# Kernel tuning notes

Measured on AMD Instinct MI355X. Metric: run time of the kernel, lower is better.

## Reference

```python
import jax, jax.numpy as jnp
import numpy as np

B, S, H, V, C = 32, 512, 256, 50000, 5
NUM_LAYERS, WINDOW = 2, 2


def setup_inputs() -> dict:
    key = jax.random.key(0)
    ks = jax.random.split(key, 24)
    std = 0.1  # matches nn.init.normal_(p, 0, 0.1)
    n = lambda k, shp: jax.random.normal(k, shp, dtype=jnp.float32) * std
    u = lambda k, shp: -0.05 + jax.random.uniform(k, shp, dtype=jnp.float32) * 0.1
    return {
        "input_sentences": jax.random.randint(ks[0], (B, S), 0, V),
        "sentences_length": jax.random.randint(ks[1], (B,), 1, S),
        "hh0": u(ks[2], (B, S, H)),
        "cs0": u(ks[3], (B, S, H)),
        "embed": n(ks[4], (V, H)),
        # stacked word-gate weights, gate order: i, l, r, f, s, output, u
        "W_lr": n(ks[5], (7, H, 2 * H)),
        "W_c": n(ks[6], (7, H, H)),
        "W_x": n(ks[7], (7, H, H)),
        "W_g": n(ks[8], (7, H, H)),
        "gate_bias": n(ks[9], (7, H)),
        # sentence-state gates
        "W_fg_g": n(ks[10], (H, H)),
        "W_fg_h": n(ks[11], (H, H)),
        "W_fgi_g": n(ks[12], (H, H)),
        "W_fgi_h": n(ks[13], (H, H)),
        "W_og_g": n(ks[14], (H, H)),
        "W_og_h": n(ks[15], (H, H)),
        "b_fg": n(ks[16], (H,)),
        "b_fgi": n(ks[17], (H,)),
        # output head
        "W1": n(ks[18], (H, 2 * H)),
        "b1": n(ks[19], (H,)),
        "Wout": n(ks[20], (C, H)),
        "bout": n(ks[21], (C,)),
    }


def _before_sum(x, window):
    # sum of right-shifted (zero-padded at front) copies, shifts 1..window
    out = jnp.zeros_like(x)
    for s in range(1, window + 1):
        out = out + jnp.pad(x[:, :-s], ((0, 0), (s, 0), (0, 0)))
    return out


def _after_sum(x, window):
    out = jnp.zeros_like(x)
    for s in range(1, window + 1):
        out = out + jnp.pad(x[:, s:], ((0, 0), (0, s), (0, 0)))
    return out


def _slstm_step(hh, cs, sv, scs, wv, W_lr, W_c, W_x, W_g, gate_bias,
                W_fg_g, W_fg_h, W_fgi_g, W_fgi_h, W_og_g, W_og_h, b_fg, b_fgi):
    avg_hh = hh.mean(axis=1)                                   # [B,H]
    f_hat_g = jax.nn.sigmoid(sv @ W_fg_g.T + avg_hh @ W_fg_h.T + b_fg)
    # NOTE: original code (faithfully) uses output_gate_bias here, not output_gate_g_bias
    og_g = jax.nn.sigmoid(sv @ W_og_g.T + avg_hh @ W_og_h.T + gate_bias[5])
    f_hat_g_i = jax.nn.sigmoid((sv @ W_fgi_g.T)[:, None] + hh @ W_fgi_h.T + b_fgi)
    scores = jax.nn.softmax(f_hat_g_i, axis=2)                 # over hidden dim
    new_scs = jax.nn.softmax(f_hat_g, axis=1) * scs + (scores * cs).sum(axis=1)
    new_sv = og_g * jnp.tanh(new_scs)

    hb = _before_sum(hh, WINDOW)
    ha = _after_sum(hh, WINDOW)
    cb = _before_sum(cs, WINDOW)
    ca = _after_sum(cs, WINDOW)
    ba = jnp.concatenate([hb, ha], axis=-1)                    # [B,S,2H]

    # all 7 gate pre-activations at once: [B,S,7,H]
    pre = (jnp.einsum('bsk,ghk->bsgh', ba, W_lr)
           + jnp.einsum('bsk,ghk->bsgh', hh, W_c)
           + jnp.einsum('bsk,ghk->bsgh', wv, W_x)
           + (jnp.einsum('bk,ghk->bgh', new_sv, W_g) + gate_bias)[:, None])

    g5 = jax.nn.sigmoid(pre[..., :5, :])                       # i,l,r,f,s
    b_, s_ = g5.shape[:2]
    # joint softmax over the concatenated 5*H gate vector (as in torch cat+softmax)
    g5 = jax.nn.softmax(g5.reshape(b_, s_, -1), axis=-1).reshape(b_, s_, 5, -1)
    i_t, l_t, r_t, f_t, s_t = (g5[..., k, :] for k in range(5))
    og = jax.nn.sigmoid(pre[..., 5, :])
    u_g = jnp.tanh(pre[..., 6, :])

    new_cs = l_t * cb + f_t * cs + r_t * ca + s_t * scs[:, None] + i_t * u_g
    new_hh = og * jnp.tanh(new_cs)
    return new_hh, new_cs, new_sv, new_scs


def reference(input_sentences, sentences_length, hh0, cs0, embed,
              W_lr, W_c, W_x, W_g, gate_bias,
              W_fg_g, W_fg_h, W_fgi_g, W_fgi_h, W_og_g, W_og_h, b_fg, b_fgi,
              W1, b1, Wout, bout):
    wv = embed[input_sentences]                                # [B,S,H]
    hh, cs = hh0, cs0
    sv, scs = hh0.mean(axis=1), cs0.mean(axis=1)
    for _ in range(NUM_LAYERS):
        hh, cs, sv, scs = _slstm_step(hh, cs, sv, scs, wv,
                                      W_lr, W_c, W_x, W_g, gate_bias,
                                      W_fg_g, W_fg_h, W_fgi_g, W_fgi_h,
                                      W_og_g, W_og_h, b_fg, b_fgi)
    avg_hh = hh.mean(axis=1)
    conc = jnp.concatenate([avg_hh, sv], axis=1) @ W1.T + b1
    fc = conc @ Wout.T + bout
    return jax.nn.log_softmax(fc, axis=1), sv
```

## Files before the change

### kernel.cpp

```cpp
#include <hip/hip_runtime.h>
#include <stdint.h>
#include <math.h>

#define B_   32
#define S_   512
#define H_   256
#define M_   (B_*S_)
#define KBIG 1024
#define NB   1792
#define C_   5

typedef __bf16 bf16;
typedef __bf16 bf16x8 __attribute__((ext_vector_type(8)));
typedef float  floatx4 __attribute__((ext_vector_type(4)));

__device__ __forceinline__ float sigm(float x){ return 1.f/(1.f+expf(-x)); }

__device__ __forceinline__ void gl16(const bf16* g, bf16* l){
    __builtin_amdgcn_global_load_lds(
        (const __attribute__((address_space(1))) unsigned int*)g,
        (__attribute__((address_space(3))) unsigned int*)l, 16, 0, 0);
}

__global__ void wcomb_k(const float* __restrict__ Wlr, const float* __restrict__ Wc,
                        const float* __restrict__ Wx, bf16* __restrict__ WT){
    int n = blockIdx.x;
    int g = n >> 8, h = n & 255;
    int k4 = threadIdx.x * 4;
    const float* src;
    if (k4 < 512)      src = Wlr + ((size_t)(g*256 + h))*512 + k4;
    else if (k4 < 768) src = Wc  + ((size_t)(g*256 + h))*256 + (k4 - 512);
    else               src = Wx  + ((size_t)(g*256 + h))*256 + (k4 - 768);
    float4 v = *(const float4*)src;
    bf16 o[4] = {(bf16)v.x,(bf16)v.y,(bf16)v.z,(bf16)v.w};
    *(uint2*)&WT[(size_t)n*KBIG + k4] = *(uint2*)o;
}

__global__ void cvtw_k(const float* __restrict__ a, bf16* __restrict__ o){
    int i4 = (blockIdx.x*256 + threadIdx.x)*4;
    float4 v = *(const float4*)(a + i4);
    bf16 t[4] = {(bf16)v.x,(bf16)v.y,(bf16)v.z,(bf16)v.w};
    *(uint2*)(o + i4) = *(uint2*)t;
}

__global__ void gather_k(const int* __restrict__ idx, const float* __restrict__ embed,
                         bf16* __restrict__ wv){
    int i4 = (blockIdx.x*256 + threadIdx.x)*4;
    int m = i4 >> 8, h = i4 & 255;
    float4 v = *(const float4*)(embed + (size_t)idx[m]*H_ + h);
    bf16 o[4] = {(bf16)v.x,(bf16)v.y,(bf16)v.z,(bf16)v.w};
    *(uint2*)(wv + (size_t)m*H_ + h) = *(uint2*)o;
}

__global__ void mean1_k(const float* __restrict__ x, float* __restrict__ part){
    int b = blockIdx.x, c = blockIdx.y, h = threadIdx.x;
    const float* p = x + ((size_t)b*S_ + c*32)*H_ + h;
    float s = 0.f;
    #pragma unroll 8
    for (int t=0;t<32;t++) s += p[(size_t)t*H_];
    part[((size_t)b*16 + c)*H_ + h] = s;
}
__global__ void mean2_k(const float* __restrict__ part, float* __restrict__ out){
    int b = blockIdx.x, h = threadIdx.x;
    float s = 0.f;
    #pragma unroll
    for (int c=0;c<16;c++) s += part[((size_t)b*16 + c)*H_ + h];
    out[b*H_ + h] = s * (1.f/512.f);
}

__global__ void buildx_k(const float* __restrict__ hh, const bf16* __restrict__ wv,
                         bf16* __restrict__ X){
    int m = blockIdx.x, h = threadIdx.x;
    int s = m & (S_-1);
    size_t base = (size_t)m*H_ + h;
    float hb = (s>=1    ? hh[base - H_] : 0.f) + (s>=2    ? hh[base - 2*H_] : 0.f);
    float ha = (s<=S_-2 ? hh[base + H_] : 0.f) + (s<=S_-3 ? hh[base + 2*H_] : 0.f);
    bf16* xr = X + (size_t)m*KBIG;
    xr[h]     = (bf16)hb;
    xr[256+h] = (bf16)ha;
    xr[512+h] = (bf16)hh[base];
    xr[768+h] = wv[base];
}

__global__ void mv5_k(const float* __restrict__ sv, const float* __restrict__ avg,
    const float* __restrict__ Wfg_g, const float* __restrict__ Wfg_h,
    const float* __restrict__ Wog_g, const float* __restrict__ Wog_h,
    const float* __restrict__ Wfgi_g, float* __restrict__ res){
    int j = blockIdx.x, b = blockIdx.y, h = threadIdx.x;
    const float* vec = (j==1 || j==3) ? avg + b*H_ : sv + b*H_;
    const float* W   = (j==0)?Wfg_g:(j==1)?Wfg_h:(j==2)?Wog_g:(j==3)?Wog_h:Wfgi_g;
    __shared__ float v[H_];
    v[h] = vec[h]; __syncthreads();
    const float* w = W + (size_t)h*H_;
    float d = 0.f;
    for (int k=0;k<H_;k++) d += v[k]*w[k];
    res[((size_t)b*5 + j)*H_ + h] = d;
}
__global__ void comb_k(const float* __restrict__ res, const float* __restrict__ b_fg,
                       const float* __restrict__ gbias, const float* __restrict__ b_fgi,
                       float* __restrict__ fhg, float* __restrict__ ogg,
                       float* __restrict__ svg){
    int b = blockIdx.x, h = threadIdx.x;
    const float* r = res + (size_t)b*5*H_;
    fhg[b*H_+h] = sigm(r[h] + r[H_+h] + b_fg[h]);
    ogg[b*H_+h] = sigm(r[2*H_+h] + r[3*H_+h] + gbias[5*H_+h]);
    svg[b*H_+h] = r[4*H_+h] + b_fgi[h];
}

template<int EPI>
__global__ __launch_bounds__(256)
void mgemm_k(const bf16* __restrict__ A, const bf16* __restrict__ BT,
             bf16* __restrict__ C, const float* __restrict__ gt,
             int Kdim, int lda, int ldb, int ldc){
    __shared__ alignas(16) bf16 lsA[128*32];
    __shared__ alignas(16) bf16 lsB[128*32];
    int tid  = threadIdx.x;
    int m0 = blockIdx.y * 128, n0 = blockIdx.x * 128;
    int wave = tid >> 6, lane = tid & 63;
    int wm = (wave & 1) * 64, wn = (wave >> 1) * 64;
    int lrow = lane & 15, quad = lane >> 4;

    floatx4 zero = {0.f,0.f,0.f,0.f};
    floatx4 acc[4][4];
    #pragma unroll
    for (int i=0;i<4;i++)
        #pragma unroll
        for (int j=0;j<4;j++) acc[i][j] = zero;

    int srow = tid >> 2;
    int scol = (tid & 3) * 8;
    const bf16* Abase = A  + (size_t)(m0 + srow)*lda + scol;
    const bf16* Bbase = BT + (size_t)(n0 + srow)*ldb + scol;
    bf16* dA0 = &lsA[srow*32 + scol];
    bf16* dA1 = &lsA[(64+srow)*32 + scol];
    bf16* dB0 = &lsB[srow*32 + scol];
    bf16* dB1 = &lsB[(64+srow)*32 + scol];

    for (int k0 = 0; k0 < Kdim; k0 += 32){
        __syncthreads();
        gl16(Abase + k0,                     dA0);
        gl16(Abase + (size_t)64*lda + k0,    dA1);
        gl16(Bbase + k0,                     dB0);
        gl16(Bbase + (size_t)64*ldb + k0,    dB1);
        __syncthreads();
        bf16x8 af[4], bfr[4];
        #pragma unroll
        for (int mi=0;mi<4;mi++) af[mi]  = *(const bf16x8*)&lsA[(wm+mi*16+lrow)*32 + quad*8];
        #pragma unroll
        for (int ni=0;ni<4;ni++) bfr[ni] = *(const bf16x8*)&lsB[(wn+ni*16+lrow)*32 + quad*8];
        #pragma unroll
        for (int mi=0;mi<4;mi++)
            #pragma unroll
            for (int ni=0;ni<4;ni++)
                acc[mi][ni] = __builtin_amdgcn_mfma_f32_16x16x32_bf16(af[mi], bfr[ni], acc[mi][ni], 0, 0, 0);
    }

    #pragma unroll
    for (int mi=0;mi<4;mi++)
        #pragma unroll
        for (int ni=0;ni<4;ni++){
            int row = m0 + wm + mi*16 + quad*4;
            int col = n0 + wn + ni*16 + lrow;
            #pragma unroll
            for (int r=0;r<4;r++){
                float v = acc[mi][ni][r];
                if (EPI) v += gt[(size_t)((row+r)>>9)*NB + col];
                C[(size_t)(row+r)*ldc + col] = (bf16)v;
            }
        }
}

template<int EPI>
__device__ __forceinline__ void mmq(floatx4 (&acc)[8][4], bf16x8 (&af)[4][2], bf16x8 (&bfr)[2][2],
                                    int MH, int NH){
    #pragma unroll
    for (int mi2=0;mi2<4;mi2++)
        #pragma unroll
        for (int ni2=0;ni2<2;ni2++)
            #pragma unroll
            for (int kk=0;kk<2;kk++)
                acc[MH*4+mi2][NH*2+ni2] = __builtin_amdgcn_mfma_f32_16x16x32_bf16(
                    af[mi2][kk], bfr[ni2][kk], acc[MH*4+mi2][NH*2+ni2], 0, 0, 0);
}

template<int EPI>
__global__ __launch_bounds__(512, 2)
void mgemm256_k(const bf16* __restrict__ A, const bf16* __restrict__ BT,
                bf16* __restrict__ C, const float* __restrict__ gt,
                int Kdim, int lda, int ldb, int ldc){
    __shared__ alignas(16) bf16 lsA[2][256*64];
    __shared__ alignas(16) bf16 lsB[2][256*64];
    const int tid  = threadIdx.x;
    const int lane = tid & 63;
    const int wave = tid >> 6;
    const int wm = wave >> 2;
    const int wn = wave & 3;
    const int lrow = lane & 15, quad = lane >> 4;
    const int m0 = blockIdx.y * 256, n0 = blockIdx.x * 256;

    const int srow = tid >> 3;
    const int scol = ((tid & 7) ^ (srow & 7)) * 8;
    const bf16* Ab = A  + (size_t)(m0 + srow)*lda + scol;
    const bf16* Bb = BT + (size_t)(n0 + srow)*ldb + scol;
    const int NT = Kdim >> 6;

    floatx4 zero = {0.f,0.f,0.f,0.f};
    floatx4 acc[8][4];
    #pragma unroll
    for (int i=0;i<8;i++)
        #pragma unroll
        for (int j=0;j<4;j++) acc[i][j] = zero;
    bf16x8 af[4][2], bfr[2][2];

#define SA_(bu,r,kt) gl16(Ab + (size_t)(r)*64*lda + (size_t)(kt)*64, &lsA[bu][(r)*4096 + tid*8])
#define SB_(bu,r,kt) gl16(Bb + (size_t)(r)*64*ldb + (size_t)(kt)*64, &lsB[bu][(r)*4096 + tid*8])
#define RA_(bu,MH,mi2,kk) (*(const bf16x8*)&lsA[bu][(wm*128 + (MH)*64 + (mi2)*16 + lrow)*64 + ((((kk)*4+quad) ^ (lrow&7))*8)])
#define RB_(bu,NH,ni2,kk) (*(const bf16x8*)&lsB[bu][(wn*64  + (NH)*32 + (ni2)*16 + lrow)*64 + ((((kk)*4+quad) ^ (lrow&7))*8)])

    SB_(0,0,0); SB_(0,1,0); SB_(0,2,0); SB_(0,3,0);
    SA_(0,0,0); SA_(0,2,0); SA_(0,1,0); SA_(0,3,0);
    asm volatile("s_waitcnt vmcnt(2)" ::: "memory");
    __builtin_amdgcn_s_barrier();

    #pragma unroll 2
    for (int kt = 0; kt < NT; ++kt){
        const int cur = kt & 1, nxt = cur ^ 1;
        const bool st = (kt + 1 < NT);
        const int k1 = kt + 1;

        if (st){ SB_(nxt,0,k1); SB_(nxt,1,k1); }
        #pragma unroll
        for (int mi2=0;mi2<4;mi2++){ af[mi2][0] = RA_(cur,0,mi2,0); af[mi2][1] = RA_(cur,0,mi2,1); }
        #pragma unroll
        for (int ni2=0;ni2<2;ni2++){ bfr[ni2][0] = RB_(cur,0,ni2,0); bfr[ni2][1] = RB_(cur,0,ni2,1); }
        __builtin_amdgcn_s_barrier();
        __builtin_amdgcn_s_setprio(1);
        mmq<EPI>(acc, af, bfr, 0, 0);
        __builtin_amdgcn_s_setprio(0);
        __builtin_amdgcn_s_barrier();

        if (st){ SB_(nxt,2,k1); SB_(nxt,3,k1); }
        #pragma unroll
        for (int ni2=0;ni2<2;ni2++){ bfr[ni2][0] = RB_(cur,1,ni2,0); bfr[ni2][1] = RB_(cur,1,ni2,1); }
        __builtin_amdgcn_s_barrier();
        __builtin_amdgcn_s_setprio(1);
        mmq<EPI>(acc, af, bfr, 0, 1);
        __builtin_amdgcn_s_setprio(0);
        if (st) asm volatile("s_waitcnt vmcnt(4)" ::: "memory");
        else    asm volatile("s_waitcnt vmcnt(0)" ::: "memory");
        __builtin_amdgcn_s_barrier();

        if (st){ SA_(nxt,0,k1); SA_(nxt,2,k1); }
        #pragma unroll
        for (int mi2=0;mi2<4;mi2++){ af[mi2][0] = RA_(cur,1,mi2,0); af[mi2][1] = RA_(cur,1,mi2,1); }
        __builtin_amdgcn_s_barrier();
        __builtin_amdgcn_s_setprio(1);
        mmq<EPI>(acc, af, bfr, 1, 1);
        __builtin_amdgcn_s_setprio(0);
        __builtin_amdgcn_s_barrier();

        if (st){ SA_(nxt,1,k1); SA_(nxt,3,k1); }
        #pragma unroll
        for (int ni2=0;ni2<2;ni2++){ bfr[ni2][0] = RB_(cur,0,ni2,0); bfr[ni2][1] = RB_(cur,0,ni2,1); }
        __builtin_amdgcn_s_barrier();
        __builtin_amdgcn_s_setprio(1);
        mmq<EPI>(acc, af, bfr, 1, 0);
        __builtin_amdgcn_s_setprio(0);
        asm volatile("s_waitcnt vmcnt(2)" ::: "memory");
        __builtin_amdgcn_s_barrier();
    }
#undef SA_
#undef SB_
#undef RA_
#undef RB_

    float gtv[4] = {0.f,0.f,0.f,0.f};
    if (EPI){
        const int b = m0 >> 9;
        #pragma unroll
        for (int ni=0;ni<4;ni++)
            gtv[ni] = gt[(size_t)b*NB + n0 + wn*64 + ni*16 + lrow];
    }
    #pragma unroll
    for (int mi=0;mi<8;mi++)
        #pragma unroll
        for (int ni=0;ni<4;ni++){
            int row = m0 + wm*128 + mi*16 + quad*4;
            int col = n0 + wn*64  + ni*16 + lrow;
            #pragma unroll
            for (int r=0;r<4;r++){
                float v = acc[mi][ni][r];
                if (EPI) v += gtv[ni];
                C[(size_t)(row+r)*ldc + col] = (bf16)v;
            }
        }
}

__global__ void scorep_k(const bf16* __restrict__ fgih, const float* __restrict__ svg,
                         const float* __restrict__ cs, float* __restrict__ part){
    int chunk = blockIdx.x, b = blockIdx.y;
    int tid = threadIdx.x, wave = tid >> 6, lane = tid & 63;
    __shared__ float acc4[4][256];
    float sw[4], acc[4] = {0.f,0.f,0.f,0.f};
    #pragma unroll
    for (int j=0;j<4;j++) sw[j] = svg[b*H_ + lane + 64*j];
    for (int t=wave; t<16; t+=4){
        int m = b*S_ + chunk*16 + t;
        const bf16* fr = fgih + (size_t)m*H_;
        float e[4], loc = 0.f;
        #pragma unroll
        for (int j=0;j<4;j++){ e[j] = expf(sigm(sw[j] + (float)fr[lane+64*j])); loc += e[j]; }
        #pragma unroll
        for (int off=32; off; off>>=1) loc += __shfl_xor(loc, off, 64);
        float inv = 1.f/loc;
        const float* cr = cs + (size_t)m*H_;
        #pragma unroll
        for (int j=0;j<4;j++) acc[j] += e[j]*inv*cr[lane+64*j];
    }
    #pragma unroll
    for (int j=0;j<4;j++) acc4[wave][lane+64*j] = acc[j];
    __syncthreads();
    part[((size_t)b*32 + chunk)*H_ + tid] =
        acc4[0][tid] + acc4[1][tid] + acc4[2][tid] + acc4[3][tid];
}

__global__ void newscs_k(const float* __restrict__ part, const float* __restrict__ fhg,
                         const float* __restrict__ ogg, const float* __restrict__ scs_in,
                         float* __restrict__ scs_out, float* __restrict__ sv_out){
    int b = blockIdx.x, h = threadIdx.x;
    __shared__ float r[256];
    float dot = 0.f;
    #pragma unroll 8
    for (int c=0;c<32;c++) dot += part[((size_t)b*32+c)*H_ + h];
    float e = expf(fhg[b*H_+h]);
    r[h] = e; __syncthreads();
    for (int off=128; off; off>>=1){ if (h<off) r[h] += r[h+off]; __syncthreads(); }
    float ns = (e / r[0]) * scs_in[b*H_+h] + dot;
    scs_out[b*H_+h] = ns;
    sv_out[b*H_+h]  = ogg[b*H_+h] * tanhf(ns);
}

__global__ void gterm_k(const float* __restrict__ svn, const float* __restrict__ Wg,
                        const float* __restrict__ gbias, float* __restrict__ gt){
    int g = blockIdx.x, b = blockIdx.y, h = threadIdx.x;
    __shared__ float s[H_];
    s[h] = svn[b*H_+h]; __syncthreads();
    const float* w = Wg + ((size_t)g*H_ + h)*H_;
    float d = 0.f;
    for (int k=0;k<H_;k++) d += s[k]*w[k];
    gt[(size_t)b*NB + g*H_ + h] = d + gbias[g*H_+h];
}

__global__ void gates_k(const bf16* __restrict__ pre, const float* __restrict__ cs_in,
                        const float* __restrict__ scs_in,
                        float* __restrict__ hh_out, float* __restrict__ cs_out){
    int tid = threadIdx.x, wave = tid >> 6, lane = tid & 63;
    int m = blockIdx.x*4 + wave;
    int b = m >> 9, s = m & (S_-1);
    const bf16* row = pre + (size_t)m*NB;
    float ex[4][5], og[4], u[4];
    float loc = 0.f;
    #pragma unroll
    for (int j=0;j<4;j++){
        int h = lane + 64*j;
        #pragma unroll
        for (int g=0; g<5; ++g){
            float e = expf(sigm((float)row[g*H_ + h]));
            ex[j][g] = e; loc += e;
        }
        og[j] = sigm((float)row[5*H_ + h]);
        u[j]  = tanhf((float)row[6*H_ + h]);
    }
    #pragma unroll
    for (int off=32; off; off>>=1) loc += __shfl_xor(loc, off, 64);
    float inv = 1.f / loc;
    #pragma unroll
    for (int j=0;j<4;j++){
        int h = lane + 64*j;
        size_t i = (size_t)m*H_ + h;
        float cb = (s>=1    ? cs_in[i - H_] : 0.f) + (s>=2    ? cs_in[i - 2*H_] : 0.f);
        float ca = (s<=S_-2 ? cs_in[i + H_] : 0.f) + (s<=S_-3 ? cs_in[i + 2*H_] : 0.f);
        float nc = ex[j][1]*inv*cb + ex[j][3]*inv*cs_in[i] + ex[j][2]*inv*ca
                 + ex[j][4]*inv*scs_in[b*H_+h] + ex[j][0]*inv*u[j];
        cs_out[i] = nc;
        hh_out[i] = og[j] * tanhf(nc);
    }
}

__global__ void head_k(const float* __restrict__ avgh, const float* __restrict__ sv,
                       const float* __restrict__ W1, const float* __restrict__ b1,
                       const float* __restrict__ Wout, const float* __restrict__ bout,
                       float* __restrict__ out){
    int b = blockIdx.x, t = threadIdx.x;
    __shared__ float conc[H_];
    __shared__ float fc[8];
    const float* wr = W1 + (size_t)t*512;
    float d = b1[t];
    for (int k=0;k<H_;k++) d += avgh[b*H_+k]*wr[k];
    for (int k=0;k<H_;k++) d += sv[b*H_+k]*wr[256+k];
    conc[t] = d;
    __syncthreads();
    if (t < C_){
        const float* wo = Wout + (size_t)t*H_;
        float s = bout[t];
        for (int i=0;i<H_;i++) s += conc[i]*wo[i];
        fc[t] = s;
    }
    __syncthreads();
    if (t == 0){
        float mx = fc[0];
        for (int c=1;c<C_;c++) mx = fmaxf(mx, fc[c]);
        float se = 0.f;
        for (int c=0;c<C_;c++) se += expf(fc[c]-mx);
        float lse = mx + logf(se);
        for (int c=0;c<C_;c++) out[b*C_+c] = fc[c]-lse;
    }
    out[B_*C_ + b*H_ + t] = sv[b*H_+t];
}

extern "C" void kernel_launch(void* const* d_in, const int* in_sizes, int n_in,
                              void* d_out, int out_size, void* d_ws, size_t ws_size,
                              hipStream_t stream){
    const int*   idx    = (const int*)d_in[0];
    const float* hh0    = (const float*)d_in[2];
    const float* cs0    = (const float*)d_in[3];
    const float* embed  = (const float*)d_in[4];
    const float* Wlr    = (const float*)d_in[5];
    const float* Wc     = (const float*)d_in[6];
    const float* Wx     = (const float*)d_in[7];
    const float* Wg     = (const float*)d_in[8];
    const float* gbias  = (const float*)d_in[9];
    const float* Wfg_g  = (const float*)d_in[10];
    const float* Wfg_h  = (const float*)d_in[11];
    const float* Wfgi_g = (const float*)d_in[12];
    const float* Wfgi_h = (const float*)d_in[13];
    const float* Wog_g  = (const float*)d_in[14];
    const float* Wog_h  = (const float*)d_in[15];
    const float* b_fg   = (const float*)d_in[16];
    const float* b_fgi  = (const float*)d_in[17];
    const float* W1     = (const float*)d_in[18];
    const float* b1     = (const float*)d_in[19];
    const float* Wout   = (const float*)d_in[20];
    const float* bout   = (const float*)d_in[21];

    uint8_t* p = (uint8_t*)d_ws;
    auto alloc = [&](size_t bytes)->void*{ void* r=(void*)p; p += (bytes + 255) & ~(size_t)255; return r; };
    bf16*  WT    = (bf16*)alloc((size_t)NB*KBIG*2);
    bf16*  WfgiT = (bf16*)alloc((size_t)H_*H_*2);
    bf16*  X     = (bf16*)alloc((size_t)M_*KBIG*2);
    bf16*  wv    = (bf16*)alloc((size_t)M_*H_*2);
    bf16*  pre   = (bf16*)alloc((size_t)M_*NB*2);
    bf16*  fgih  = (bf16*)alloc((size_t)M_*H_*2);
    float* hhA = (float*)alloc((size_t)M_*H_*4);
    float* csA = (float*)alloc((size_t)M_*H_*4);
    float* hhB = (float*)alloc((size_t)M_*H_*4);
    float* csB = (float*)alloc((size_t)M_*H_*4);
    float* mpart= (float*)alloc((size_t)B_*16*H_*4);
    float* part = (float*)alloc((size_t)B_*32*H_*4);
    float* res5 = (float*)alloc((size_t)B_*5*H_*4);
    float* avgh = (float*)alloc(B_*H_*4);
    float* fhg  = (float*)alloc(B_*H_*4);
    float* ogg  = (float*)alloc(B_*H_*4);
    float* svg  = (float*)alloc(B_*H_*4);
    float* svP0 = (float*)alloc(B_*H_*4);
    float* svP1 = (float*)alloc(B_*H_*4);
    float* scP0 = (float*)alloc(B_*H_*4);
    float* scP1 = (float*)alloc(B_*H_*4);
    float* gt   = (float*)alloc((size_t)B_*NB*4);

    wcomb_k <<<NB,          256, 0, stream>>>(Wlr, Wc, Wx, WT);
    cvtw_k  <<<(H_*H_)/1024,256, 0, stream>>>(Wfgi_h, WfgiT);
    gather_k<<<(M_*H_)/1024,256, 0, stream>>>(idx, embed, wv);
    mean1_k <<<dim3(B_,16), 256, 0, stream>>>(hh0, mpart);
    mean2_k <<<B_,          256, 0, stream>>>(mpart, svP0);
    mean1_k <<<dim3(B_,16), 256, 0, stream>>>(cs0, mpart);
    mean2_k <<<B_,          256, 0, stream>>>(mpart, scP0);

    const float *hin = hh0, *cin = cs0;
    float *hout = hhA, *cout = csA;
    float *svin = svP0, *scin = scP0, *svout = svP1, *scout = scP1;

    for (int l=0; l<2; ++l){
        const float* avgp;
        if (l == 0){
            avgp = svin;
        } else {
            mean1_k<<<dim3(B_,16), 256, 0, stream>>>(hin, mpart);
            mean2_k<<<B_,          256, 0, stream>>>(mpart, avgh);
            avgp = avgh;
        }
        mv5_k   <<<dim3(5,B_), 256, 0, stream>>>(svin, avgp, Wfg_g, Wfg_h, Wog_g,
                                                 Wog_h, Wfgi_g, res5);
        comb_k  <<<B_, 256, 0, stream>>>(res5, b_fg, gbias, b_fgi, fhg, ogg, svg);
        buildx_k<<<M_, 256, 0, stream>>>(hin, wv, X);
        mgemm_k<0><<<dim3(2,128), 256, 0, stream>>>(X+512, WfgiT, fgih, nullptr,
                                                    H_, KBIG, H_, H_);
        scorep_k<<<dim3(32,B_), 256, 0, stream>>>(fgih, svg, cin, part);
        newscs_k<<<B_, 256, 0, stream>>>(part, fhg, ogg, scin, scout, svout);
        gterm_k <<<dim3(7,B_), 256, 0, stream>>>(svout, Wg, gbias, gt);
        mgemm256_k<1><<<dim3(7,64), 512, 0, stream>>>(X, WT, pre, gt,
                                                      KBIG, KBIG, KBIG, NB);
        gates_k <<<M_/4, 256, 0, stream>>>(pre, cin, scin, hout, cout);
        hin = hout; cin = cout;
        hout = (l==0) ? hhB : hhA;
        cout = (l==0) ? csB : csA;
        float* q;
        q = svin; svin = svout; svout = q;
        q = scin; scin = scout; scout = q;
    }
    mean1_k<<<dim3(B_,16), 256, 0, stream>>>(hin, mpart);
    mean2_k<<<B_,          256, 0, stream>>>(mpart, avgh);
    head_k <<<B_, 256, 0, stream>>>(avgh, svin, W1, b1, Wout, bout, (float*)d_out);
}
```

Baseline: 594.2 us.

## Vectorize buildx and gates kernels, remap GEMM blocks across XCDs, hoist prefetches

buildx_k and gates_k now load and store four elements per thread with float4 and bf16x4 accesses instead of scalar strided ones, which cuts the number of memory instructions. The big GEMM switches to a 1D grid with an XCD-aware remap (8 chunks) so neighbouring tiles share L2. It also issues all next-tile global-to-LDS loads at the top of each k-iteration, with adjusted waitcnts and no unroll pragma. Issuing all loads up front may raise in-flight pressure and shift how MFMA overlaps with loads.

```diff
diff --git a/kernel.cpp b/kernel.cpp
--- a/kernel.cpp
+++ b/kernel.cpp
@@ -11,6 +11,7 @@
 #define C_   5
 
 typedef __bf16 bf16;
+typedef __bf16 bf16x4 __attribute__((ext_vector_type(4)));
 typedef __bf16 bf16x8 __attribute__((ext_vector_type(8)));
 typedef float  floatx4 __attribute__((ext_vector_type(4)));
 
@@ -70,16 +71,31 @@
 
 __global__ void buildx_k(const float* __restrict__ hh, const bf16* __restrict__ wv,
                          bf16* __restrict__ X){
-    int m = blockIdx.x, h = threadIdx.x;
+    int m = blockIdx.x, tid = threadIdx.x;
+    int seg = tid >> 6, li = tid & 63;
     int s = m & (S_-1);
-    size_t base = (size_t)m*H_ + h;
-    float hb = (s>=1    ? hh[base - H_] : 0.f) + (s>=2    ? hh[base - 2*H_] : 0.f);
-    float ha = (s<=S_-2 ? hh[base + H_] : 0.f) + (s<=S_-3 ? hh[base + 2*H_] : 0.f);
-    bf16* xr = X + (size_t)m*KBIG;
-    xr[h]     = (bf16)hb;
-    xr[256+h] = (bf16)ha;
-    xr[512+h] = (bf16)hh[base];
-    xr[768+h] = wv[base];
+    int h0 = li*4;
+    size_t base = (size_t)m*H_ + h0;
+    bf16* xr = X + (size_t)m*KBIG + seg*H_ + h0;
+    const float4 z = {0.f,0.f,0.f,0.f};
+    if (seg == 3){
+        *(uint2*)xr = *(const uint2*)&wv[base];
+        return;
+    }
+    float4 v;
+    if (seg == 0){
+        float4 a = (s>=1) ? *(const float4*)&hh[base - H_]   : z;
+        float4 b = (s>=2) ? *(const float4*)&hh[base - 2*H_] : z;
+        v.x=a.x+b.x; v.y=a.y+b.y; v.z=a.z+b.z; v.w=a.w+b.w;
+    } else if (seg == 1){
+        float4 a = (s<=S_-2) ? *(const float4*)&hh[base + H_]   : z;
+        float4 b = (s<=S_-3) ? *(const float4*)&hh[base + 2*H_] : z;
+        v.x=a.x+b.x; v.y=a.y+b.y; v.z=a.z+b.z; v.w=a.w+b.w;
+    } else {
+        v = *(const float4*)&hh[base];
+    }
+    bf16 o[4] = {(bf16)v.x,(bf16)v.y,(bf16)v.z,(bf16)v.w};
+    *(uint2*)xr = *(uint2*)o;
 }
 
 __global__ void mv5_k(const float* __restrict__ sv, const float* __restrict__ avg,
@@ -187,7 +203,7 @@
 __global__ __launch_bounds__(512, 2)
 void mgemm256_k(const bf16* __restrict__ A, const bf16* __restrict__ BT,
                 bf16* __restrict__ C, const float* __restrict__ gt,
-                int Kdim, int lda, int ldb, int ldc){
+                int Kdim, int lda, int ldb, int ldc, int nbx){
     __shared__ alignas(16) bf16 lsA[2][256*64];
     __shared__ alignas(16) bf16 lsB[2][256*64];
     const int tid  = threadIdx.x;
@@ -196,7 +212,12 @@
     const int wm = wave >> 2;
     const int wn = wave & 3;
     const int lrow = lane & 15, quad = lane >> 4;
-    const int m0 = blockIdx.y * 256, n0 = blockIdx.x * 256;
+
+    const int nwg = gridDim.x;
+    const int cpx = nwg >> 3;
+    const int w   = (blockIdx.x & 7)*cpx + (blockIdx.x >> 3);
+    const int mb  = w / nbx, nb = w - mb*nbx;
+    const int m0 = mb * 256, n0 = nb * 256;
 
     const int srow = tid >> 3;
     const int scol = ((tid & 7) ^ (srow & 7)) * 8;
@@ -222,13 +243,16 @@
     asm volatile("s_waitcnt vmcnt(2)" ::: "memory");
     __builtin_amdgcn_s_barrier();
 
-    #pragma unroll 2
     for (int kt = 0; kt < NT; ++kt){
         const int cur = kt & 1, nxt = cur ^ 1;
         const bool st = (kt + 1 < NT);
         const int k1 = kt + 1;
 
-        if (st){ SB_(nxt,0,k1); SB_(nxt,1,k1); }
+        if (st){
+            SB_(nxt,0,k1); SB_(nxt,1,k1); SB_(nxt,2,k1); SB_(nxt,3,k1);
+            SA_(nxt,0,k1); SA_(nxt,2,k1); SA_(nxt,1,k1); SA_(nxt,3,k1);
+        }
+
         #pragma unroll
         for (int mi2=0;mi2<4;mi2++){ af[mi2][0] = RA_(cur,0,mi2,0); af[mi2][1] = RA_(cur,0,mi2,1); }
         #pragma unroll
@@ -239,18 +263,16 @@
         __builtin_amdgcn_s_setprio(0);
         __builtin_amdgcn_s_barrier();
 
-        if (st){ SB_(nxt,2,k1); SB_(nxt,3,k1); }
         #pragma unroll
         for (int ni2=0;ni2<2;ni2++){ bfr[ni2][0] = RB_(cur,1,ni2,0); bfr[ni2][1] = RB_(cur,1,ni2,1); }
         __builtin_amdgcn_s_barrier();
         __builtin_amdgcn_s_setprio(1);
         mmq<EPI>(acc, af, bfr, 0, 1);
         __builtin_amdgcn_s_setprio(0);
-        if (st) asm volatile("s_waitcnt vmcnt(4)" ::: "memory");
+        if (st) asm volatile("s_waitcnt vmcnt(8)" ::: "memory");
         else    asm volatile("s_waitcnt vmcnt(0)" ::: "memory");
         __builtin_amdgcn_s_barrier();
 
-        if (st){ SA_(nxt,0,k1); SA_(nxt,2,k1); }
         #pragma unroll
         for (int mi2=0;mi2<4;mi2++){ af[mi2][0] = RA_(cur,1,mi2,0); af[mi2][1] = RA_(cur,1,mi2,1); }
         __builtin_amdgcn_s_barrier();
@@ -259,14 +281,13 @@
         __builtin_amdgcn_s_setprio(0);
         __builtin_amdgcn_s_barrier();
 
-        if (st){ SA_(nxt,1,k1); SA_(nxt,3,k1); }
         #pragma unroll
         for (int ni2=0;ni2<2;ni2++){ bfr[ni2][0] = RB_(cur,0,ni2,0); bfr[ni2][1] = RB_(cur,0,ni2,1); }
         __builtin_amdgcn_s_barrier();
         __builtin_amdgcn_s_setprio(1);
         mmq<EPI>(acc, af, bfr, 1, 0);
         __builtin_amdgcn_s_setprio(0);
-        asm volatile("s_waitcnt vmcnt(2)" ::: "memory");
+        if (st) asm volatile("s_waitcnt vmcnt(2)" ::: "memory");
         __builtin_amdgcn_s_barrier();
     }
 #undef SA_
@@ -358,33 +379,46 @@
     int m = blockIdx.x*4 + wave;
     int b = m >> 9, s = m & (S_-1);
     const bf16* row = pre + (size_t)m*NB;
-    float ex[4][5], og[4], u[4];
+    int h0 = lane*4;
+    float pv[7][4];
+    #pragma unroll
+    for (int g=0; g<7; ++g){
+        bf16x4 t = *(const bf16x4*)&row[g*H_ + h0];
+        #pragma unroll
+        for (int j=0;j<4;j++) pv[g][j] = (float)t[j];
+    }
+    float ex[5][4], og[4], u[4];
     float loc = 0.f;
     #pragma unroll
-    for (int j=0;j<4;j++){
-        int h = lane + 64*j;
-        #pragma unroll
-        for (int g=0; g<5; ++g){
-            float e = expf(sigm((float)row[g*H_ + h]));
-            ex[j][g] = e; loc += e;
-        }
-        og[j] = sigm((float)row[5*H_ + h]);
-        u[j]  = tanhf((float)row[6*H_ + h]);
-    }
+    for (int g=0; g<5; ++g)
+        #pragma unroll
+        for (int j=0;j<4;j++){ float e = expf(sigm(pv[g][j])); ex[g][j] = e; loc += e; }
+    #pragma unroll
+    for (int j=0;j<4;j++){ og[j] = sigm(pv[5][j]); u[j] = tanhf(pv[6][j]); }
     #pragma unroll
     for (int off=32; off; off>>=1) loc += __shfl_xor(loc, off, 64);
     float inv = 1.f / loc;
+
+    size_t i0 = (size_t)m*H_ + h0;
+    const float4 z = {0.f,0.f,0.f,0.f};
+    float4 c0  = *(const float4*)&cs_in[i0];
+    float4 cm1 = (s>=1)    ? *(const float4*)&cs_in[i0 - H_]   : z;
+    float4 cm2 = (s>=2)    ? *(const float4*)&cs_in[i0 - 2*H_] : z;
+    float4 cp1 = (s<=S_-2) ? *(const float4*)&cs_in[i0 + H_]   : z;
+    float4 cp2 = (s<=S_-3) ? *(const float4*)&cs_in[i0 + 2*H_] : z;
+    float4 sc  = *(const float4*)&scs_in[(size_t)b*H_ + h0];
+    float4 nc4, nh4;
     #pragma unroll
     for (int j=0;j<4;j++){
-        int h = lane + 64*j;
-        size_t i = (size_t)m*H_ + h;
-        float cb = (s>=1    ? cs_in[i - H_] : 0.f) + (s>=2    ? cs_in[i - 2*H_] : 0.f);
-        float ca = (s<=S_-2 ? cs_in[i + H_] : 0.f) + (s<=S_-3 ? cs_in[i + 2*H_] : 0.f);
-        float nc = ex[j][1]*inv*cb + ex[j][3]*inv*cs_in[i] + ex[j][2]*inv*ca
-                 + ex[j][4]*inv*scs_in[b*H_+h] + ex[j][0]*inv*u[j];
-        cs_out[i] = nc;
-        hh_out[i] = og[j] * tanhf(nc);
-    }
+        float cb = ((const float*)&cm1)[j] + ((const float*)&cm2)[j];
+        float ca = ((const float*)&cp1)[j] + ((const float*)&cp2)[j];
+        float nc = ex[1][j]*inv*cb + ex[3][j]*inv*((const float*)&c0)[j] + ex[2][j]*inv*ca
+                 + ex[4][j]*inv*((const float*)&sc)[j] + ex[0][j]*inv*u[j];
+        ((float*)&nc4)[j] = nc;
+        ((float*)&nh4)[j] = og[j] * tanhf(nc);
+    }
+    *(float4*)&cs_out[i0] = nc4;
+    *(float4*)&hh_out[i0] = nh4;
 }
 
 __global__ void head_k(const float* __restrict__ avgh, const float* __restrict__ sv,
@@ -498,8 +532,8 @@
         scorep_k<<<dim3(32,B_), 256, 0, stream>>>(fgih, svg, cin, part);
         newscs_k<<<B_, 256, 0, stream>>>(part, fhg, ogg, scin, scout, svout);
         gterm_k <<<dim3(7,B_), 256, 0, stream>>>(svout, Wg, gbias, gt);
-        mgemm256_k<1><<<dim3(7,64), 512, 0, stream>>>(X, WT, pre, gt,
-                                                      KBIG, KBIG, KBIG, NB);
+        mgemm256_k<1><<<448, 512, 0, stream>>>(X, WT, pre, gt,
+                                               KBIG, KBIG, KBIG, NB, 7);
         gates_k <<<M_/4, 256, 0, stream>>>(pre, cin, scin, hout, cout);
         hin = hout; cin = cout;
         hout = (l==0) ? hhB : hhA;
```

Result: faster. 554.0 us (-6.8%).
